# Kernel tuning notes

Hardware: AMD Instinct MI355X
Metric: run time of the kernel (lower is better)

Reference implementation:

```python
import jax, jax.numpy as jnp
import numpy as np

N, H, DK, DV, DFF, D = 2, 8, 32, 32, 512, 256
B, S = 2, 2048
MASK_VALUE = -1e-30
EPS = 1e-14  # K.epsilon()**2 with default epsilon 1e-7


def glorot(key, shape):
    fan_in, fan_out = shape[-2], shape[-1]
    limit = np.sqrt(6.0 / (fan_in + fan_out))
    return jax.random.uniform(key, shape, jnp.float32, -limit, limit)


def setup_inputs() -> dict:
    key = jax.random.key(0)
    ks = jax.random.split(key, 8)
    return {
        "x": jax.random.normal(ks[0], (B, S, D), jnp.float32),
        "mask": jnp.ones((B, S), jnp.float32),
        "Wq": glorot(ks[1], (N, H, D, DK)),
        "Wk": glorot(ks[2], (N, H, D, DK)),
        "Wv": glorot(ks[3], (N, H, D, DV)),
        "Wo": glorot(ks[4], (N, H * DV, D)),
        "W1": glorot(ks[5], (N, D, DFF)),
        "b1": jnp.zeros((N, DFF), jnp.float32),
        "W2": glorot(ks[6], (N, DFF, D)),
        "b2": jnp.zeros((N, D), jnp.float32),
        "gamma": jnp.ones((2 * N,), jnp.float32),
        "beta": jnp.zeros((2 * N,), jnp.float32),
    }


def _layernorm(x, g, b):
    mean = jnp.mean(x, axis=-1, keepdims=True)
    var = jnp.mean(jnp.square(x - mean), axis=-1, keepdims=True)
    return (x - mean) / jnp.sqrt(var + EPS) * g + b


def reference(x, mask, Wq, Wk, Wv, Wo, W1, b1, W2, b2, gamma, beta):
    m = mask[:, None, None, :]  # [B,1,1,S], multiplies score rows' key axis
    for i in range(N):
        # batched multi-head attention (no 1/sqrt(dk) scaling, faithful to source)
        q = jnp.einsum("bsd,hdk->bhsk", x, Wq[i])
        k = jnp.einsum("bsd,hdk->bhsk", x, Wk[i])
        v = jnp.einsum("bsd,hdv->bhsv", x, Wv[i])
        A = jnp.einsum("bhsk,bhtk->bhst", q, k)  # [B,H,S,S]
        A = m * A + (1.0 - m) * MASK_VALUE
        A = jax.nn.softmax(A, axis=-1)
        o = jnp.einsum("bhst,bhtv->bhsv", A, v)
        conc = o.transpose(0, 2, 1, 3).reshape(x.shape[0], x.shape[1], H * DV)
        x = x + conc @ Wo[i]
        x = _layernorm(x, gamma[2 * i], beta[2 * i])
        ffn = jax.nn.relu(x @ W1[i] + b1[i]) @ W2[i] + b2[i]
        x = x + ffn
        x = _layernorm(x, gamma[2 * i + 1], beta[2 * i + 1])
    return x
```

## Files before the change

kernel.cpp:

```cpp
#include <hip/hip_runtime.h>
#include <hip/hip_bf16.h>

#define NL 2
#define NH 8
#define DKk 32
#define DVv 32
#define DFF 512
#define DD 256
#define BB 2
#define SS 2048
#define MROWS (BB*SS)
#define LN_EPS 1e-14f
#define L2E 1.4426950408889634f
#define SOFT_SHIFT_L2E (50.0f*L2E)

typedef __hip_bfloat16 bf16;
typedef unsigned short us;
typedef short bf16x8 __attribute__((ext_vector_type(8)));
typedef float f32x4  __attribute__((ext_vector_type(4)));
typedef unsigned short us4 __attribute__((ext_vector_type(4)));

#define O_XF   256
#define O_QB   (O_XF+1048576)
#define O_KH   (O_QB+1048576)
#define O_KL   (O_KH+524288)
#define O_VT   (O_KL+524288)
#define O_XH   (O_VT+524288)
#define O_XL   (O_XH+524288)
#define O_OP   (O_XL+524288)
#define O_ML   (O_OP+2097152)
#define O_MASK (O_ML+65536)
#define O_B1   (O_MASK+4096)
#define O_B2   (O_B1+1024)
#define O_GM   (O_B2+512)
#define O_BT   (O_GM+4)
#define O_PREP (O_BT+4)
#define CONV_TOTAL (1048576+4096+1024+512+4+4)
#define CONV_BLOCKS ((CONV_TOTAL+255)/256)
#define PREP_BLOCKS 512
#define PQH 0u
#define PQL 393216u
#define POH 786432u
#define POL 917504u
#define P1H 1048576u
#define P1L 1310720u
#define P2H 1572864u
#define P2L 1835008u

__device__ __forceinline__ float us2f(us u){
  unsigned int v = ((unsigned int)u) << 16; float f;
  __builtin_memcpy(&f, &v, 4); return f;
}
__device__ __forceinline__ us f2bf_rne(float f){
  unsigned int b = __float_as_uint(f);
  b += 0x7FFFu + ((b>>16)&1u);
  return (us)(b>>16);
}

#if __has_builtin(__builtin_amdgcn_exp2f)
#define EXP2F(x) __builtin_amdgcn_exp2f(x)
#else
#define EXP2F(x) exp2f(x)
#endif

#if __has_builtin(__builtin_amdgcn_cvt_pk_bf16_f32)
typedef __bf16 bf16x2_t __attribute__((ext_vector_type(2)));
__device__ __forceinline__ int pack_bf16(float a, float b){
  bf16x2_t r = __builtin_amdgcn_cvt_pk_bf16_f32(a, b);
  int i; __builtin_memcpy(&i, &r, 4); return i;
}
#else
__device__ __forceinline__ int pack_bf16(float a, float b){
  int b0 = __float_as_int(a) + 0x8000;
  int b1 = __float_as_int(b) + 0x8000;
  return (b1 & 0xFFFF0000) | ((int)((unsigned)b0 >> 16));
}
#endif

__device__ __forceinline__ void gl_lds16(const us* g, us* l){
  __builtin_amdgcn_global_load_lds(
    (const __attribute__((address_space(1))) unsigned int*)g,
    (__attribute__((address_space(3))) unsigned int*)l, 16, 0, 0);
}

__device__ __forceinline__ size_t xhl_idx(int row, int col){
  int rt = row>>6, rg = (row>>4)&3, L15 = row&15;
  int kc = col>>5, Q = (col>>3)&3, j = col&7;
  return ((size_t)(rt*8+kc))*2048 + rg*512 + Q*128 + L15*8 + j;
}

__device__ __forceinline__ float conv1(const void* src, size_t i, int flag){
  if(flag) return ((const float*)src)[i];
  return us2f(((const us*)src)[i]);
}

__device__ __forceinline__ void prep_b_raw(const void* W0, const void* W1v, const void* W2v,
                                           int baseoff, us* __restrict__ Bh, us* __restrict__ Bl,
                                           int Kd, int Nd, int qkv, int g, int flag)
{
  int total = (Kd/32)*(Nd/16)*64;
  if(g >= total) return;
  int lane = g & 63, fi = g >> 6;
  int ncN = Nd/16;
  int nc = fi % ncN, kc = fi / ncN;
  int Q = lane>>4, L15 = lane&15;
  int n = nc*16 + L15;
  const void* src;
  int off0, stride;
  if(qkv){
    int sec = n>>8, h = (n>>5)&7, kq = n&31;
    src = (sec==0)?W0:((sec==1)?W1v:W2v);
    off0 = baseoff + h*8192 + kq;
    stride = 32;
  } else {
    src = W0;
    off0 = baseoff + n;
    stride = Nd;
  }
  #pragma unroll
  for(int j=0;j<8;j++){
    int k = kc*32 + Q*8 + j;
    float v = conv1(src, (size_t)off0 + (size_t)k*stride, flag);
    us hb = f2bf_rne(v);
    Bh[(size_t)g*8 + j] = hb;
    Bl[(size_t)g*8 + j] = f2bf_rne(v - us2f(hb));
  }
}

__global__ void conv_prep(const void* s0, const void* s1, const void* sWq, const void* sWk,
                          const void* sWv, const void* sWo, const void* sW1, const void* sb1,
                          const void* sW2, const void* sb2, const void* sgm, const void* sbt,
                          float* __restrict__ ws, int* __restrict__ flagp)
{
  __shared__ int fsh[4];
  int bad = 0;
  const us* xr = (const us*)s0;
  for(int i=threadIdx.x; i<4096; i+=256){
    float f = us2f(xr[i]);
    if(!(fabsf(f) < 1e3f)) bad = 1;
  }
  unsigned long long m = __ballot(bad);
  if((threadIdx.x&63)==0) fsh[threadIdx.x>>6] = (m!=0ull);
  __syncthreads();
  int flag = (fsh[0]|fsh[1]|fsh[2]|fsh[3]);
  if(blockIdx.x==0 && threadIdx.x==0) *flagp = flag;

  int b = blockIdx.x;
  if(b < PREP_BLOCKS){
    int layer = b >> 8, lb = b & 255;
    us* prep = (us*)(ws + O_PREP);
    if(lb < 96){
      int g = lb*256 + threadIdx.x;
      prep_b_raw(sWq, sWk, sWv, layer*65536, prep+PQH+(size_t)layer*196608,
                 prep+PQL+(size_t)layer*196608, 256, 768, 1, g, flag);
    } else if(lb < 128){
      int g = (lb-96)*256 + threadIdx.x;
      prep_b_raw(sWo, nullptr, nullptr, layer*65536, prep+POH+(size_t)layer*65536,
                 prep+POL+(size_t)layer*65536, 256, 256, 0, g, flag);
    } else if(lb < 192){
      int g = (lb-128)*256 + threadIdx.x;
      prep_b_raw(sW1, nullptr, nullptr, layer*131072, prep+P1H+(size_t)layer*131072,
                 prep+P1L+(size_t)layer*131072, 256, 512, 0, g, flag);
    } else {
      int g = (lb-192)*256 + threadIdx.x;
      prep_b_raw(sW2, nullptr, nullptr, layer*131072, prep+P2H+(size_t)layer*131072,
                 prep+P2L+(size_t)layer*131072, 512, 256, 0, g, flag);
    }
    return;
  }
  int g = (b - PREP_BLOCKS)*256 + threadIdx.x;
  if(g < 1048576){
    float v = conv1(s0, g, flag);
    ws[O_XF+g] = v;
    us hb = f2bf_rne(v);
    us lb = f2bf_rne(v - us2f(hb));
    size_t xi = xhl_idx(g>>8, g&255);
    ((us*)(ws+O_XH))[xi] = hb;
    ((us*)(ws+O_XL))[xi] = lb;
    return;
  }
  g -= 1048576;
  if(g < 4096){ ws[O_MASK+g] = conv1(s1, g, flag)*L2E; return; }
  g -= 4096;
  if(g < 1024){ ws[O_B1+g] = conv1(sb1, g, flag); return; }
  g -= 1024;
  if(g < 512){ ws[O_B2+g] = conv1(sb2, g, flag); return; }
  g -= 512;
  if(g < 4){ ws[O_GM+g] = conv1(sgm, g, flag); return; }
  g -= 4;
  if(g < 4){ ws[O_BT+g] = conv1(sbt, g, flag); return; }
}

template<int MODE>
__launch_bounds__(256)
__global__ void gemm_mfma(const us* __restrict__ Axh, const us* __restrict__ Axl,
                          const us* __restrict__ Bh, const us* __restrict__ Bl,
                          const float* __restrict__ bias,
                          float* __restrict__ O,
                          us* __restrict__ QH, us* __restrict__ QL,
                          us* __restrict__ KH, us* __restrict__ KL, us* __restrict__ VT,
                          int Ncols, int Kdim)
{
  __shared__ __align__(16) us SH[9216];
  us* Ah = SH; us* Al = SH+2048; us* Bhs = SH+4096; us* Bls = SH+6144;
  const int t = threadIdx.x;
  const int w = t>>6, lane = t&63;
  const int Q = lane>>4, L15 = lane&15;
  const int row0 = blockIdx.x*64;
  const int nc0 = blockIdx.y*4;
  const int col0 = blockIdx.y*64;

  f32x4 acc[2][2];
  #pragma unroll
  for(int i=0;i<2;i++)
    #pragma unroll
    for(int j=0;j<2;j++) acc[i][j] = (f32x4){0.f,0.f,0.f,0.f};

  const int nKc = Kdim>>5;
  const int ncW = Ncols>>4;

  for(int kc=0; kc<nKc; kc++){
    {
      size_t abase = ((size_t)(blockIdx.x*nKc + kc))*2048;
      gl_lds16(&Axh[abase + (size_t)t*8], &Ah[t*8]);
      gl_lds16(&Axl[abase + (size_t)t*8], &Al[t*8]);
      size_t gidx = ((size_t)(kc*ncW + nc0 + w)*64 + lane)*8;
      gl_lds16(&Bh[gidx], &Bhs[t*8]);
      gl_lds16(&Bl[gidx], &Bls[t*8]);
    }
    __syncthreads();

    bf16x8 aAh[2], aAl[2], bBh[2], bBl[2];
    #pragma unroll
    for(int rg2=0;rg2<2;rg2++){
      int rg = (w&1)*2 + rg2;
      aAh[rg2] = *(const bf16x8*)&Ah[rg*512 + lane*8];
      aAl[rg2] = *(const bf16x8*)&Al[rg*512 + lane*8];
    }
    #pragma unroll
    for(int cg2=0;cg2<2;cg2++){
      int nc = (w>>1)*2 + cg2;
      bBh[cg2] = *(const bf16x8*)&Bhs[nc*512 + lane*8];
      bBl[cg2] = *(const bf16x8*)&Bls[nc*512 + lane*8];
    }
    #pragma unroll
    for(int rg2=0;rg2<2;rg2++)
      #pragma unroll
      for(int cg2=0;cg2<2;cg2++){
        acc[rg2][cg2] = __builtin_amdgcn_mfma_f32_16x16x32_bf16(aAl[rg2], bBh[cg2], acc[rg2][cg2], 0,0,0);
        acc[rg2][cg2] = __builtin_amdgcn_mfma_f32_16x16x32_bf16(aAh[rg2], bBl[cg2], acc[rg2][cg2], 0,0,0);
        acc[rg2][cg2] = __builtin_amdgcn_mfma_f32_16x16x32_bf16(aAh[rg2], bBh[cg2], acc[rg2][cg2], 0,0,0);
      }
    __syncthreads();
  }

  if(MODE==0){
    us* TH = SH;
    us* TL = SH + 4608;
    #pragma unroll
    for(int rg2=0;rg2<2;rg2++)
      #pragma unroll
      for(int cg2=0;cg2<2;cg2++)
        #pragma unroll
        for(int r=0;r<4;r++){
          int rl = (w&1)*32 + rg2*16 + Q*4 + r;
          int cl = (w>>1)*32 + cg2*16 + L15;
          float va = acc[rg2][cg2][r];
          us hb = f2bf_rne(va);
          TH[rl*72+cl] = hb;
          TL[rl*72+cl] = f2bf_rne(va - us2f(hb));
        }
    __syncthreads();
    const int sec = col0>>8;
    const int h0  = (col0&255)>>5;
    const int b_  = row0>>11;
    const int srow0 = row0 & 2047;
    if(sec < 2){
      us* DH = (sec==0) ? QH : KH;
      us* DL = (sec==0) ? QL : KL;
      #pragma unroll
      for(int u2=0; u2<2; u2++){
        int u = w + u2*4;
        int rg = u&3, half = u>>2;
        int lbase = (rg*16 + L15)*72 + half*32 + Q*8;
        bf16x8 hv = *(const bf16x8*)&TH[lbase];
        bf16x8 lv = *(const bf16x8*)&TL[lbase];
        int bh = b_*NH + h0 + half;
        size_t dbase = ((size_t)(bh*128 + (srow0>>4) + rg)*64 + lane)*8;
        *(bf16x8*)&DH[dbase] = hv;
        *(bf16x8*)&DL[dbase] = lv;
      }
    } else {
      #pragma unroll
      for(int u2=0; u2<2; u2++){
        int u = w + u2*4;
        int sgrp = u&1, kqh = (u>>1)&1, half = u>>2;
        union{ us u8[8]; bf16x8 v; } vv;
        #pragma unroll
        for(int j=0;j<8;j++){
          int rl = sgrp*32 + Q*8 + j;
          int cl = half*32 + kqh*16 + L15;
          vv.u8[j] = TH[rl*72+cl];
        }
        int bh = b_*NH + h0 + half;
        size_t dbase = ((size_t)((bh*64 + (srow0>>5) + sgrp)*2 + kqh)*64 + lane)*8;
        *(bf16x8*)&VT[dbase] = vv.v;
      }
    }
  } else {
    #pragma unroll
    for(int rg2=0;rg2<2;rg2++)
      #pragma unroll
      for(int cg2=0;cg2<2;cg2++)
        #pragma unroll
        for(int r=0;r<4;r++){
          int row = row0 + (w&1)*32 + rg2*16 + Q*4 + r;
          int c   = col0 + (w>>1)*32 + cg2*16 + L15;
          float v = acc[rg2][cg2][r] + bias[c];
          O[(size_t)row*Ncols + c] = v>0.f ? v : 0.f;
        }
  }
}

template<int SRC>
__launch_bounds__(256)
__global__ void gemm_ln(const float* __restrict__ A,
                        const float* __restrict__ OpartA, const float* __restrict__ MLA,
                        const us* __restrict__ Bh, const us* __restrict__ Bl,
                        const float* __restrict__ bias, const float* __restrict__ res,
                        float* __restrict__ xf,
                        us* __restrict__ xh, us* __restrict__ xl,
                        const float* __restrict__ gamma, const float* __restrict__ beta, int gi,
                        void* __restrict__ out, int write_out,
                        const int* __restrict__ flagp, int Kdim)
{
  __shared__ __align__(16) us Ah[512], Al[512];
  __shared__ __align__(16) us Bhs[8192], Bls[8192];
  __shared__ float lred[128];
  const int t = threadIdx.x;
  const int w = t>>6, lane = t&63;
  const int Q = lane>>4, L15 = lane&15;
  const int row0 = blockIdx.x*16;
  const int nKc = Kdim>>5;

  f32x4 acc[4];
  #pragma unroll
  for(int cg=0;cg<4;cg++) acc[cg] = (f32x4){0.f,0.f,0.f,0.f};

  for(int kc=0; kc<nKc; kc++){
    if(t < 128){
      int r = t>>3;
      int kl = (t&7)*4;
      float4 v;
      if(SRC==0){
        int row = row0 + r;
        int b_ = row>>11, s_ = row&2047;
        size_t i0 = (size_t)(b_*8 + kc)*2048 + s_;
        float l = MLA[i0] + MLA[i0+32768];
        float inv = 1.f/l;
        float4 o0 = *(const float4*)&OpartA[i0*32 + kl];
        float4 o1 = *(const float4*)&OpartA[(i0+32768)*32 + kl];
        v.x=(o0.x+o1.x)*inv; v.y=(o0.y+o1.y)*inv;
        v.z=(o0.z+o1.z)*inv; v.w=(o0.w+o1.w)*inv;
      } else {
        v = *(const float4*)&A[(size_t)(row0+r)*Kdim + kc*32 + kl];
      }
      float f[4] = {v.x, v.y, v.z, v.w};
      us4 h4, l4;
      #pragma unroll
      for(int j=0;j<4;j++){
        us hb = f2bf_rne(f[j]);
        h4[j] = hb; l4[j] = f2bf_rne(f[j] - us2f(hb));
      }
      int off = (kl>>3)*128 + r*8 + (kl&7);
      *(us4*)&Ah[off] = h4;
      *(us4*)&Al[off] = l4;
    }
    #pragma unroll
    for(int ii=0; ii<4; ii++){
      int unit = w + ii*4;
      size_t gidx = ((size_t)(kc*16 + unit)*64 + lane)*8;
      gl_lds16(&Bh[gidx], &Bhs[unit*512 + lane*8]);
      gl_lds16(&Bl[gidx], &Bls[unit*512 + lane*8]);
    }
    __syncthreads();

    bf16x8 aAh = *(const bf16x8*)&Ah[lane*8];
    bf16x8 aAl = *(const bf16x8*)&Al[lane*8];
    #pragma unroll
    for(int cg=0;cg<4;cg++){
      int unit = w*4 + cg;
      bf16x8 bBh = *(const bf16x8*)&Bhs[unit*512 + lane*8];
      bf16x8 bBl = *(const bf16x8*)&Bls[unit*512 + lane*8];
      acc[cg] = __builtin_amdgcn_mfma_f32_16x16x32_bf16(aAl, bBh, acc[cg], 0,0,0);
      acc[cg] = __builtin_amdgcn_mfma_f32_16x16x32_bf16(aAh, bBl, acc[cg], 0,0,0);
      acc[cg] = __builtin_amdgcn_mfma_f32_16x16x32_bf16(aAh, bBh, acc[cg], 0,0,0);
    }
    __syncthreads();
  }

  float tmp[4][4];
  #pragma unroll
  for(int cg=0;cg<4;cg++)
    #pragma unroll
    for(int r=0;r<4;r++){
      int row = row0 + Q*4 + r;
      int c = w*64 + cg*16 + L15;
      float v = acc[cg][r] + res[(size_t)row*DD + c];
      if(SRC==1) v += bias[c];
      tmp[cg][r] = v;
    }
  float s[4], sq[4];
  #pragma unroll
  for(int r=0;r<4;r++){
    s[r]  = tmp[0][r]+tmp[1][r]+tmp[2][r]+tmp[3][r];
    sq[r] = tmp[0][r]*tmp[0][r]+tmp[1][r]*tmp[1][r]+tmp[2][r]*tmp[2][r]+tmp[3][r]*tmp[3][r];
  }
  #pragma unroll
  for(int off=1; off<16; off<<=1)
    #pragma unroll
    for(int r=0;r<4;r++){
      s[r]  += __shfl_xor(s[r], off);
      sq[r] += __shfl_xor(sq[r], off);
    }
  if(L15==0){
    #pragma unroll
    for(int r=0;r<4;r++){
      int rl = Q*4 + r;
      lred[(w*16 + rl)*2]   = s[r];
      lred[(w*16 + rl)*2+1] = sq[r];
    }
  }
  __syncthreads();
  float g = gamma[gi], bb = beta[gi];
  float scv[4], mnv[4];
  #pragma unroll
  for(int r=0;r<4;r++){
    int rl = Q*4 + r;
    float S  = lred[rl*2]   + lred[(16+rl)*2]   + lred[(32+rl)*2]   + lred[(48+rl)*2];
    float SQ = lred[rl*2+1] + lred[(16+rl)*2+1] + lred[(32+rl)*2+1] + lred[(48+rl)*2+1];
    float mean = S*(1.f/DD);
    float var  = SQ*(1.f/DD) - mean*mean;
    scv[r] = rsqrtf(var+LN_EPS)*g;
    mnv[r] = mean;
  }
  int flag = write_out ? *flagp : 0;
  #pragma unroll
  for(int cg=0;cg<4;cg++)
    #pragma unroll
    for(int r=0;r<4;r++){
      int row = row0 + Q*4 + r;
      int c = w*64 + cg*16 + L15;
      float val = (tmp[cg][r]-mnv[r])*scv[r] + bb;
      xf[(size_t)row*DD + c] = val;
      us hb = f2bf_rne(val);
      size_t xi = xhl_idx(row, c);
      xh[xi] = hb;
      xl[xi] = f2bf_rne(val - us2f(hb));
      if(write_out){
        if(flag) ((float*)out)[(size_t)row*DD + c] = val;
        else     ((bf16*)out)[(size_t)row*DD + c] = __float2bfloat16(val);
      }
    }
}

__launch_bounds__(256)
__global__ void attn_kernel(const us* __restrict__ QH, const us* __restrict__ QL,
                            const us* __restrict__ KH, const us* __restrict__ KL,
                            const us* __restrict__ VT,
                            const float* __restrict__ mask,
                            float* __restrict__ Opart, float* __restrict__ ML)
{
  __shared__ __align__(16) us Khs[4096], Kls[4096], Vts[4096];
  __shared__ __align__(16) float Msl[128];
  const int t = threadIdx.x;
  const int bh = blockIdx.x >> 6;
  const int qt = (blockIdx.x & 63) >> 1;
  const int ks = blockIdx.x & 1;
  const int b_ = bh >> 3;
  const int wv = t >> 6;
  const int lane = t & 63;
  const int Q = lane >> 4, L15 = lane & 15;
  const int q0 = qt*64 + wv*16;

  size_t qidx = ((size_t)(bh*128 + qt*4 + wv)*64 + lane)*8;
  const bf16x8 qh_v = *(const bf16x8*)&QH[qidx];
  const bf16x8 ql_v = *(const bf16x8*)&QL[qidx];

  const us* KHbh = KH + (size_t)bh*65536;
  const us* KLbh = KL + (size_t)bh*65536;
  const us* VTbh = VT + (size_t)bh*65536;
  const int base = ks*1024;

  f32x4 Oa0a = {0.f,0.f,0.f,0.f}, Oa0b = {0.f,0.f,0.f,0.f};
  f32x4 Oa1a = {0.f,0.f,0.f,0.f}, Oa1b = {0.f,0.f,0.f,0.f};
  float lacc = 0.f;

  {
    size_t kbase = (size_t)(base>>4)*512;
    size_t vbase = (size_t)(base>>5)*1024;
    gl_lds16(&KHbh[kbase + (size_t)t*8], &Khs[t*8]);
    gl_lds16(&KLbh[kbase + (size_t)t*8], &Kls[t*8]);
    gl_lds16(&VTbh[vbase + (size_t)t*8], &Vts[t*8]);
    if(t < 64) Msl[t] = mask[b_*SS + base + t];
  }

  for(int s=0; s<16; s++){
    __syncthreads();
    if(s < 15){
      int t0n = base + (s+1)*64;
      int bn = (s+1)&1;
      size_t kbase = (size_t)(t0n>>4)*512;
      size_t vbase = (size_t)(t0n>>5)*1024;
      gl_lds16(&KHbh[kbase + (size_t)t*8], &Khs[bn*2048 + t*8]);
      gl_lds16(&KLbh[kbase + (size_t)t*8], &Kls[bn*2048 + t*8]);
      gl_lds16(&VTbh[vbase + (size_t)t*8], &Vts[bn*2048 + t*8]);
      if(t < 64) Msl[bn*64 + t] = mask[b_*SS + t0n + t];
    }
    const int bo = (s&1)*2048;
    const int mo = (s&1)*64;

    f32x4 St[4];
    const f32x4 zz = {0.f,0.f,0.f,0.f};
    #pragma unroll
    for(int kt=0;kt<4;kt++){
      bf16x8 aKh = *(const bf16x8*)&Khs[bo + kt*512 + lane*8];
      bf16x8 aKl = *(const bf16x8*)&Kls[bo + kt*512 + lane*8];
      f32x4 a = __builtin_amdgcn_mfma_f32_16x16x32_bf16(aKl, qh_v, zz, 0,0,0);
      a = __builtin_amdgcn_mfma_f32_16x16x32_bf16(aKh, ql_v, a, 0,0,0);
      a = __builtin_amdgcn_mfma_f32_16x16x32_bf16(aKh, qh_v, a, 0,0,0);
      St[kt] = a;
    }

    float lsum = 0.f;
    #pragma unroll
    for(int kt=0;kt<4;kt++){
      float4 mv = *(const float4*)&Msl[mo + kt*16 + Q*4];
      float mvr[4] = {mv.x, mv.y, mv.z, mv.w};
      #pragma unroll
      for(int r=0;r<4;r++){
        float p = EXP2F(fmaf(mvr[r], St[kt][r], -SOFT_SHIFT_L2E));
        St[kt][r] = p;
        lsum += p;
      }
    }
    lacc += lsum;

    int pk[4][2];
    #pragma unroll
    for(int kt=0;kt<4;kt++){
      pk[kt][0] = pack_bf16(St[kt][0], St[kt][1]);
      pk[kt][1] = pack_bf16(St[kt][2], St[kt][3]);
    }

    #pragma unroll
    for(int c=0;c<2;c++){
      union { int i[4]; bf16x8 v; } bu;
      #pragma unroll
      for(int d=0;d<4;d++){
        int srcl = (((Q&1)*2 + (d>>1))<<4) | L15;
        int vlo = __shfl(pk[2*c  ][d&1], srcl, 64);
        int vhi = __shfl(pk[2*c+1][d&1], srcl, 64);
        bu.i[d] = (Q & 2) ? vhi : vlo;
      }
      bf16x8 aV0 = *(const bf16x8*)&Vts[bo + (c*2+0)*512 + lane*8];
      bf16x8 aV1 = *(const bf16x8*)&Vts[bo + (c*2+1)*512 + lane*8];
      if(c == 0){
        Oa0a = __builtin_amdgcn_mfma_f32_16x16x32_bf16(aV0, bu.v, Oa0a, 0,0,0);
        Oa1a = __builtin_amdgcn_mfma_f32_16x16x32_bf16(aV1, bu.v, Oa1a, 0,0,0);
      } else {
        Oa0b = __builtin_amdgcn_mfma_f32_16x16x32_bf16(aV0, bu.v, Oa0b, 0,0,0);
        Oa1b = __builtin_amdgcn_mfma_f32_16x16x32_bf16(aV1, bu.v, Oa1b, 0,0,0);
      }
    }
  }

  f32x4 Oa0 = Oa0a + Oa0b;
  f32x4 Oa1 = Oa1a + Oa1b;
  lacc += __shfl_xor(lacc, 16);
  lacc += __shfl_xor(lacc, 32);

  float* opp = &Opart[((size_t)(ks*16+bh)*SS + q0 + L15)*32];
  #pragma unroll
  for(int r=0;r<4;r++){
    opp[Q*4+r]    = Oa0[r];
    opp[16+Q*4+r] = Oa1[r];
  }
  if(Q==0){
    ML[(size_t)(ks*16+bh)*SS + q0 + L15] = lacc;
  }
}

extern "C" void kernel_launch(void* const* d_in, const int* in_sizes, int n_in,
                              void* d_out, int out_size, void* d_ws, size_t ws_size,
                              hipStream_t stream)
{
  float* ws = (float*)d_ws;
  int* flagp = (int*)d_ws;

  float* xf  = ws + O_XF;
  us* QHb = (us*)(ws + O_QB);
  us* QLb = QHb + 1048576;
  us* KH = (us*)(ws + O_KH);
  us* KL = (us*)(ws + O_KL);
  us* VT = (us*)(ws + O_VT);
  us* XH = (us*)(ws + O_XH);
  us* XL = (us*)(ws + O_XL);
  float* Opart = ws + O_OP;
  float* ML  = ws + O_ML;
  float* fh  = Opart;
  float* b1f = ws + O_B1;
  float* b2f_ = ws + O_B2;
  float* gmf = ws + O_GM;
  float* btf = ws + O_BT;
  us* prep = (us*)(ws + O_PREP);

  conv_prep<<<PREP_BLOCKS+CONV_BLOCKS,256,0,stream>>>(
      d_in[0], d_in[1], d_in[2], d_in[3], d_in[4], d_in[5],
      d_in[6], d_in[7], d_in[8], d_in[9], d_in[10], d_in[11],
      ws, flagp);

  for(int i=0;i<NL;i++){
    const float* b1i = b1f + (size_t)i*DFF;
    const float* b2i = b2f_ + (size_t)i*DD;

    dim3 g0(64, 12);
    gemm_mfma<0><<<g0,256,0,stream>>>(XH, XL,
                                      prep+PQH+(size_t)i*196608, prep+PQL+(size_t)i*196608,
                                      nullptr, nullptr,
                                      QHb, QLb, KH, KL, VT, 768, 256);
    attn_kernel<<<1024,256,0,stream>>>(QHb, QLb, KH, KL, VT, ws + O_MASK, Opart, ML);
    gemm_ln<0><<<256,256,0,stream>>>(nullptr, Opart, ML,
                                     prep+POH+(size_t)i*65536, prep+POL+(size_t)i*65536,
                                     nullptr, xf, xf, XH, XL,
                                     gmf, btf, 2*i, d_out, 0, flagp, 256);
    dim3 g2(64, 8);
    gemm_mfma<2><<<g2,256,0,stream>>>(XH, XL,
                                      prep+P1H+(size_t)i*131072, prep+P1L+(size_t)i*131072,
                                      b1i, fh,
                                      nullptr, nullptr, nullptr, nullptr, nullptr, 512, 256);
    gemm_ln<1><<<256,256,0,stream>>>(fh, nullptr, nullptr,
                                     prep+P2H+(size_t)i*131072, prep+P2L+(size_t)i*131072,
                                     b2i, xf, xf, XH, XL,
                                     gmf, btf, 2*i+1, d_out, (i==NL-1)?1:0, flagp, 512);
  }
}
```

Before: 269.4 us.

## Double-buffer LDS staging in MFMA GEMM kernels to overlap loads with compute

```diff
diff --git a/kernel.cpp b/kernel.cpp
--- a/kernel.cpp
+++ b/kernel.cpp
@@ -201,34 +201,43 @@
                           us* __restrict__ KH, us* __restrict__ KL, us* __restrict__ VT,
                           int Ncols, int Kdim)
 {
-  __shared__ __align__(16) us SH[9216];
-  us* Ah = SH; us* Al = SH+2048; us* Bhs = SH+4096; us* Bls = SH+6144;
+  __shared__ __align__(16) us SH[16384];
   const int t = threadIdx.x;
   const int w = t>>6, lane = t&63;
   const int Q = lane>>4, L15 = lane&15;
-  const int row0 = blockIdx.x*64;
-  const int nc0 = blockIdx.y*4;
-  const int col0 = blockIdx.y*64;
-
-  f32x4 acc[2][2];
-  #pragma unroll
-  for(int i=0;i<2;i++)
-    #pragma unroll
-    for(int j=0;j<2;j++) acc[i][j] = (f32x4){0.f,0.f,0.f,0.f};
-
+  const int bx = blockIdx.x, by = blockIdx.y;
+  const int row0 = bx*64;
+  const int nc0 = by*4;
+  const int col0 = by*64;
   const int nKc = Kdim>>5;
   const int ncW = Ncols>>4;
 
+  f32x4 acc[2][2];
+  #pragma unroll
+  for(int i=0;i<2;i++)
+    #pragma unroll
+    for(int j=0;j<2;j++) acc[i][j] = (f32x4){0.f,0.f,0.f,0.f};
+
+  auto stage = [&](int kc){
+    const int bo = (kc&1)*8192;
+    size_t abase = ((size_t)(bx*nKc + kc))*2048;
+    gl_lds16(&Axh[abase + (size_t)t*8], &SH[bo + t*8]);
+    gl_lds16(&Axl[abase + (size_t)t*8], &SH[bo + 2048 + t*8]);
+    size_t gidx = ((size_t)(kc*ncW + nc0 + w)*64 + lane)*8;
+    gl_lds16(&Bh[gidx], &SH[bo + 4096 + t*8]);
+    gl_lds16(&Bl[gidx], &SH[bo + 6144 + t*8]);
+  };
+
+  stage(0);
+
   for(int kc=0; kc<nKc; kc++){
-    {
-      size_t abase = ((size_t)(blockIdx.x*nKc + kc))*2048;
-      gl_lds16(&Axh[abase + (size_t)t*8], &Ah[t*8]);
-      gl_lds16(&Axl[abase + (size_t)t*8], &Al[t*8]);
-      size_t gidx = ((size_t)(kc*ncW + nc0 + w)*64 + lane)*8;
-      gl_lds16(&Bh[gidx], &Bhs[t*8]);
-      gl_lds16(&Bl[gidx], &Bls[t*8]);
-    }
     __syncthreads();
+    if(kc+1 < nKc) stage(kc+1);
+    const int bo = (kc&1)*8192;
+    const us* Ah  = SH + bo;
+    const us* Al  = SH + bo + 2048;
+    const us* Bhs = SH + bo + 4096;
+    const us* Bls = SH + bo + 6144;
 
     bf16x8 aAh[2], aAl[2], bBh[2], bBl[2];
     #pragma unroll
@@ -251,10 +260,10 @@
         acc[rg2][cg2] = __builtin_amdgcn_mfma_f32_16x16x32_bf16(aAh[rg2], bBl[cg2], acc[rg2][cg2], 0,0,0);
         acc[rg2][cg2] = __builtin_amdgcn_mfma_f32_16x16x32_bf16(aAh[rg2], bBh[cg2], acc[rg2][cg2], 0,0,0);
       }
+  }
+
+  if(MODE==0){
     __syncthreads();
-  }
-
-  if(MODE==0){
     us* TH = SH;
     us* TL = SH + 4608;
     #pragma unroll
@@ -334,8 +343,8 @@
                         void* __restrict__ out, int write_out,
                         const int* __restrict__ flagp, int Kdim)
 {
-  __shared__ __align__(16) us Ah[512], Al[512];
-  __shared__ __align__(16) us Bhs[8192], Bls[8192];
+  __shared__ __align__(16) us Ahs[1024], Als[1024];
+  __shared__ __align__(16) us Bhs[16384], Bls[16384];
   __shared__ float lred[128];
   const int t = threadIdx.x;
   const int w = t>>6, lane = t&63;
@@ -347,56 +356,84 @@
   #pragma unroll
   for(int cg=0;cg<4;cg++) acc[cg] = (f32x4){0.f,0.f,0.f,0.f};
 
-  for(int kc=0; kc<nKc; kc++){
+  float4 pv0, pv1, pv;
+  float pl0 = 0.f, pl1 = 0.f;
+
+  auto preloadA = [&](int kc){
     if(t < 128){
       int r = t>>3;
       int kl = (t&7)*4;
-      float4 v;
       if(SRC==0){
         int row = row0 + r;
         int b_ = row>>11, s_ = row&2047;
         size_t i0 = (size_t)(b_*8 + kc)*2048 + s_;
-        float l = MLA[i0] + MLA[i0+32768];
-        float inv = 1.f/l;
-        float4 o0 = *(const float4*)&OpartA[i0*32 + kl];
-        float4 o1 = *(const float4*)&OpartA[(i0+32768)*32 + kl];
-        v.x=(o0.x+o1.x)*inv; v.y=(o0.y+o1.y)*inv;
-        v.z=(o0.z+o1.z)*inv; v.w=(o0.w+o1.w)*inv;
+        pl0 = MLA[i0];
+        pl1 = MLA[i0+32768];
+        pv0 = *(const float4*)&OpartA[i0*32 + kl];
+        pv1 = *(const float4*)&OpartA[(i0+32768)*32 + kl];
       } else {
-        v = *(const float4*)&A[(size_t)(row0+r)*Kdim + kc*32 + kl];
-      }
-      float f[4] = {v.x, v.y, v.z, v.w};
+        pv = *(const float4*)&A[(size_t)(row0+r)*Kdim + kc*32 + kl];
+      }
+    }
+  };
+  auto writeA = [&](int kc){
+    if(t < 128){
+      int r = t>>3;
+      int kl = (t&7)*4;
+      float f[4];
+      if(SRC==0){
+        float inv = 1.f/(pl0 + pl1);
+        f[0]=(pv0.x+pv1.x)*inv; f[1]=(pv0.y+pv1.y)*inv;
+        f[2]=(pv0.z+pv1.z)*inv; f[3]=(pv0.w+pv1.w)*inv;
+      } else {
+        f[0]=pv.x; f[1]=pv.y; f[2]=pv.z; f[3]=pv.w;
+      }
       us4 h4, l4;
       #pragma unroll
       for(int j=0;j<4;j++){
         us hb = f2bf_rne(f[j]);
         h4[j] = hb; l4[j] = f2bf_rne(f[j] - us2f(hb));
       }
+      int bo = (kc&1)*512;
       int off = (kl>>3)*128 + r*8 + (kl&7);
-      *(us4*)&Ah[off] = h4;
-      *(us4*)&Al[off] = l4;
-    }
+      *(us4*)&Ahs[bo+off] = h4;
+      *(us4*)&Als[bo+off] = l4;
+    }
+  };
+  auto stageB = [&](int kc){
+    const int bo = (kc&1)*8192;
     #pragma unroll
     for(int ii=0; ii<4; ii++){
       int unit = w + ii*4;
       size_t gidx = ((size_t)(kc*16 + unit)*64 + lane)*8;
-      gl_lds16(&Bh[gidx], &Bhs[unit*512 + lane*8]);
-      gl_lds16(&Bl[gidx], &Bls[unit*512 + lane*8]);
-    }
+      gl_lds16(&Bh[gidx], &Bhs[bo + unit*512 + lane*8]);
+      gl_lds16(&Bl[gidx], &Bls[bo + unit*512 + lane*8]);
+    }
+  };
+
+  preloadA(0);
+  stageB(0);
+  writeA(0);
+
+  for(int kc=0; kc<nKc; kc++){
     __syncthreads();
-
-    bf16x8 aAh = *(const bf16x8*)&Ah[lane*8];
-    bf16x8 aAl = *(const bf16x8*)&Al[lane*8];
+    if(kc+1 < nKc){
+      preloadA(kc+1);
+      stageB(kc+1);
+    }
+    const int bo = (kc&1);
+    bf16x8 aAh = *(const bf16x8*)&Ahs[bo*512 + lane*8];
+    bf16x8 aAl = *(const bf16x8*)&Als[bo*512 + lane*8];
     #pragma unroll
     for(int cg=0;cg<4;cg++){
       int unit = w*4 + cg;
-      bf16x8 bBh = *(const bf16x8*)&Bhs[unit*512 + lane*8];
-      bf16x8 bBl = *(const bf16x8*)&Bls[unit*512 + lane*8];
+      bf16x8 bBh = *(const bf16x8*)&Bhs[bo*8192 + unit*512 + lane*8];
+      bf16x8 bBl = *(const bf16x8*)&Bls[bo*8192 + unit*512 + lane*8];
       acc[cg] = __builtin_amdgcn_mfma_f32_16x16x32_bf16(aAl, bBh, acc[cg], 0,0,0);
       acc[cg] = __builtin_amdgcn_mfma_f32_16x16x32_bf16(aAh, bBl, acc[cg], 0,0,0);
       acc[cg] = __builtin_amdgcn_mfma_f32_16x16x32_bf16(aAh, bBh, acc[cg], 0,0,0);
     }
-    __syncthreads();
+    if(kc+1 < nKc) writeA(kc+1);
   }
 
   float tmp[4][4];
```

After: 258.7 us. 1.04x faster.
